# Optimization experiments

Measured on AMD Instinct MI355X. Metric: run time of the kernel, lower is better.

Reference implementation:

```python
import jax, jax.numpy as jnp
import numpy as np

B, H, W, C = 8, 32, 32, 256
HEADS, UNITS = 8, 256
OUT_D = UNITS // HEADS          # 32
HID_D = int(OUT_D * 1.0)        # 32 (hidden_rate=1.0)


def setup_inputs() -> dict:
    key = jax.random.key(0)
    ks = jax.random.split(key, 8)
    glorot_qk = np.sqrt(6.0 / (C + HID_D)).astype(np.float32)
    glorot_v = np.sqrt(6.0 / (C + OUT_D)).astype(np.float32)
    return {
        "seq": jax.random.normal(ks[0], (B, H, W, C), dtype=jnp.float32),
        "ctx": jax.random.normal(ks[1], (B, H, W, C), dtype=jnp.float32),
        "Wq": jax.random.uniform(ks[2], (HEADS, C, HID_D), jnp.float32, -glorot_qk, glorot_qk),
        "Wk": jax.random.uniform(ks[3], (HEADS, C, HID_D), jnp.float32, -glorot_qk, glorot_qk),
        "Wv": jax.random.uniform(ks[4], (HEADS, C, OUT_D), jnp.float32, -glorot_v, glorot_v),
        "bq": jnp.zeros((HEADS, HID_D), jnp.float32),
        "bk": jnp.zeros((HEADS, HID_D), jnp.float32),
        "bv": jnp.zeros((HEADS, OUT_D), jnp.float32),
    }


def reference(seq, ctx, Wq, Wk, Wv, bq, bk, bv):
    # NB: the original layer computes q, k, v all from `seq`; `ctx` only fixes
    # the weight shapes. Dropout omitted (inference / deterministic baseline).
    b, h, w, c = seq.shape
    n = h * w
    s = seq.reshape(b, n, c)
    q = jnp.einsum("bnc,hcd->bhnd", s, Wq) + bq[None, :, None, :]
    k = jnp.einsum("bnc,hcd->bhnd", s, Wk) + bk[None, :, None, :]
    v = jnp.einsum("bnc,hcd->bhnd", s, Wv) + bv[None, :, None, :]
    scale = 1.0 / jnp.sqrt(jnp.asarray(k.shape[-1], k.dtype))
    logits = jnp.einsum("bhnd,bhmd->bhnm", q, k * scale)  # [B,heads,N,N]
    attn = jax.nn.softmax(logits, axis=-1)
    a = jnp.einsum("bhnm,bhmd->bhnd", attn, jnp.tanh(v))  # tanh on V, as in source
    out = a.transpose(0, 2, 1, 3).reshape(b, h, w, -1)     # concat heads on channel
    return out
```

## Files before the change

kernel.cpp:

```cpp
#include <hip/hip_runtime.h>
#include <hip/hip_bf16.h>

typedef __attribute__((ext_vector_type(8))) short bf16x8_t;
typedef __attribute__((ext_vector_type(4))) float f32x4_t;
typedef __attribute__((ext_vector_type(16))) float f32x16_t;
typedef __attribute__((ext_vector_type(4))) unsigned short u16x4_t;
typedef __attribute__((ext_vector_type(2))) unsigned u32x2_t;

#define DEVINL __device__ __forceinline__

static constexpr int CN   = 256;
static constexpr int NSEQ = 1024;
static constexpr int NH   = 8;
static constexpr float QSCALE = 0.17677669529663687f * 1.4426950408889634f;

DEVINL unsigned short f2bf(float f) {
    union { __hip_bfloat16 h; unsigned short u; } cv;
    cv.h = __float2bfloat16(f);
    return cv.u;
}

DEVINL unsigned cvtpk_bf16(float lo, float hi) {
    unsigned r;
    asm("v_cvt_pk_bf16_f32 %0, %1, %2" : "=v"(r) : "v"(lo), "v"(hi));
    return r;
}

DEVINL float partner32_f(float x, int h2) {
    unsigned u = __builtin_bit_cast(unsigned, x);
    u32x2_t r = __builtin_amdgcn_permlane32_swap(u, u, false, false);
    return __builtin_bit_cast(float, h2 ? r.x : r.y);
}

DEVINL float fast_tanh(float x) {
    x = fminf(fmaxf(x, -20.f), 20.f);
    float t = __builtin_amdgcn_exp2f(2.8853900817779268f * x);
    return (t - 1.f) * __builtin_amdgcn_rcpf(t + 1.f);
}

__global__ void prep_kernel(const float* __restrict__ Wq, const float* __restrict__ Wk,
                            const float* __restrict__ Wv, const float* __restrict__ seq,
                            unsigned short* __restrict__ Wbt, unsigned short* __restrict__ Sb) {
    if (blockIdx.x < 768) {
        int idx  = blockIdx.x * 256 + threadIdx.x;
        int c    = idx & 255;
        int ncol = idx >> 8;
        int h = ncol / 96, r = ncol % 96;
        int t = r >> 5, d = r & 31;
        const float* W = (t == 0) ? Wq : (t == 1) ? Wk : Wv;
        Wbt[idx] = f2bf(W[((h << 8) + c) * 32 + d]);
    } else {
        int i = (blockIdx.x - 768) * 256 + threadIdx.x;
        const float4 x = ((const float4*)seq)[2 * i];
        const float4 y = ((const float4*)seq)[2 * i + 1];
        union { unsigned u[4]; bf16x8_t v8; } rv;
        rv.u[0] = cvtpk_bf16(x.x, x.y);
        rv.u[1] = cvtpk_bf16(x.z, x.w);
        rv.u[2] = cvtpk_bf16(y.x, y.y);
        rv.u[3] = cvtpk_bf16(y.z, y.w);
        *(bf16x8_t*)(Sb + (size_t)i * 8) = rv.v8;
    }
}

__global__ __launch_bounds__(256) void proj_kernel(
        const unsigned short* __restrict__ Sb, const unsigned short* __restrict__ Wbt,
        const float* __restrict__ bq, const float* __restrict__ bk, const float* __restrict__ bv,
        unsigned short* __restrict__ Qs, unsigned short* __restrict__ Kf,
        unsigned short* __restrict__ Vf) {
    const int w    = threadIdx.x >> 6;
    const int lane = threadIdx.x & 63;
    const int l15  = lane & 15, l4 = lane >> 4;
    const int mw = blockIdx.y * 64 + (w >> 1) * 32;
    const int nw = blockIdx.x * 128 + (w & 1) * 64;

    f32x4_t acc[2][4];
    for (int mg = 0; mg < 2; ++mg)
        for (int g = 0; g < 4; ++g)
            acc[mg][g] = (f32x4_t){0.f, 0.f, 0.f, 0.f};

#pragma unroll
    for (int k0 = 0; k0 < CN; k0 += 32) {
        const int kk = k0 + l4 * 8;
        bf16x8_t a[2], b[4];
        for (int mg = 0; mg < 2; ++mg)
            a[mg] = *(const bf16x8_t*)(Sb + (size_t)(mw + mg * 16 + l15) * CN + kk);
        for (int g = 0; g < 4; ++g)
            b[g] = *(const bf16x8_t*)(Wbt + (size_t)(nw + g * 16 + l15) * CN + kk);
        for (int mg = 0; mg < 2; ++mg)
            for (int g = 0; g < 4; ++g)
                acc[mg][g] = __builtin_amdgcn_mfma_f32_16x16x32_bf16(a[mg], b[g], acc[mg][g], 0, 0, 0);
    }

    for (int g = 0; g < 4; ++g) {
        const int ncol = nw + g * 16;
        const int h = ncol / 96, r = ncol % 96;
        const int t = r >> 5;
        const int d = (r & 31) + l15;
        for (int mg = 0; mg < 2; ++mg) {
            const int m0 = mw + mg * 16 + l4 * 4;
            const int b_ = m0 >> 10;
            const int n0 = m0 & 1023;
            const int bh = b_ * NH + h;
            const int kt = n0 >> 5;
            if (t == 2) {
                const float bias = bv[h * 32 + d];
                u16x4_t vs;
                for (int i = 0; i < 4; ++i)
                    vs[i] = f2bf(fast_tanh(acc[mg][g][i] + bias));
                const size_t fidx = ((size_t)(bh * 32 + kt) * 2 + ((n0 >> 4) & 1)) * 64
                                    + d + 32 * ((n0 >> 3) & 1);
                *(u16x4_t*)(Vf + fidx * 8 + (n0 & 7)) = vs;
            } else if (t == 0) {
                const float bias = bq[h * 32 + d];
                for (int i = 0; i < 4; ++i)
                    Qs[((size_t)bh * NSEQ + n0 + i) * 32 + d] = f2bf((acc[mg][g][i] + bias) * QSCALE);
            } else {
                const float bias = bk[h * 32 + d];
                const size_t fbase = (((size_t)(bh * 32 + kt) * 2 + (d >> 4)) * 64
                                      + 32 * ((d >> 3) & 1)) * 8 + (d & 7);
                for (int i = 0; i < 4; ++i)
                    Kf[fbase + (size_t)((n0 + i) & 31) * 8] = f2bf(acc[mg][g][i] + bias);
            }
        }
    }
}

__global__ __launch_bounds__(256, 2) void attn_kernel(
        const unsigned short* __restrict__ Qs, const unsigned short* __restrict__ Kf,
        const unsigned short* __restrict__ Vf, float* __restrict__ out) {
    __shared__ float comb[2][2][64][17];
    const int lane = threadIdx.x & 63;
    const int w    = threadIdx.x >> 6;
    const int l31  = lane & 31;
    const int h2   = lane >> 5;
    const int qsel = w >> 1, ksel = w & 1;
    const int id = blockIdx.x;
    const int bh = (id & 7) + 8 * ((id >> 3) & 7);
    const int qt = id >> 6;
    const int b_ = bh >> 3, h = bh & 7;
    const int qbase = qt * 128 + qsel * 64;

    const unsigned short* Qpa = Qs + ((size_t)bh * NSEQ + qbase + l31) * 32 + h2 * 8;
    const unsigned short* Qpb = Qpa + 32 * 32;
    const bf16x8_t qf0a = *(const bf16x8_t*)(Qpa);
    const bf16x8_t qf1a = *(const bf16x8_t*)(Qpa + 16);
    const bf16x8_t qf0b = *(const bf16x8_t*)(Qpb);
    const bf16x8_t qf1b = *(const bf16x8_t*)(Qpb + 16);

    const unsigned short* Kp = Kf + (size_t)bh * 32768 + ksel * 16384 + lane * 8;
    const unsigned short* Vp = Vf + (size_t)bh * 32768 + ksel * 16384 + lane * 8;

    f32x16_t oa = {0.f,0.f,0.f,0.f,0.f,0.f,0.f,0.f,0.f,0.f,0.f,0.f,0.f,0.f,0.f,0.f};
    f32x16_t ob = {0.f,0.f,0.f,0.f,0.f,0.f,0.f,0.f,0.f,0.f,0.f,0.f,0.f,0.f,0.f,0.f};
    float la = 0.f, lb = 0.f;

    bf16x8_t kf0 = *(const bf16x8_t*)(Kp);
    bf16x8_t kf1 = *(const bf16x8_t*)(Kp + 512);
    bf16x8_t va0 = *(const bf16x8_t*)(Vp);
    bf16x8_t va1 = *(const bf16x8_t*)(Vp + 512);

#pragma unroll
    for (int kt = 0; kt < 16; ++kt) {
        const int ktn = (kt + 1) & 15;
        bf16x8_t nk0 = *(const bf16x8_t*)(Kp + ktn * 1024);
        bf16x8_t nk1 = *(const bf16x8_t*)(Kp + ktn * 1024 + 512);
        bf16x8_t nv0 = *(const bf16x8_t*)(Vp + ktn * 1024);
        bf16x8_t nv1 = *(const bf16x8_t*)(Vp + ktn * 1024 + 512);

        {
            f32x16_t st = {0.f,0.f,0.f,0.f,0.f,0.f,0.f,0.f,0.f,0.f,0.f,0.f,0.f,0.f,0.f,0.f};
            __builtin_amdgcn_s_setprio(1);
            st = __builtin_amdgcn_mfma_f32_32x32x16_bf16(kf0, qf0a, st, 0, 0, 0);
            st = __builtin_amdgcn_mfma_f32_32x32x16_bf16(kf1, qf1a, st, 0, 0, 0);
            __builtin_amdgcn_s_setprio(0);
            float p[16];
#pragma unroll
            for (int r = 0; r < 16; ++r) p[r] = __builtin_amdgcn_exp2f(st[r]);
            float s8[8];
#pragma unroll
            for (int g = 0; g < 8; ++g) s8[g] = p[2 * g] + p[2 * g + 1];
            la += ((s8[0] + s8[1]) + (s8[2] + s8[3])) + ((s8[4] + s8[5]) + (s8[6] + s8[7]));
            unsigned pw[8];
#pragma unroll
            for (int g = 0; g < 8; ++g) pw[g] = cvtpk_bf16(p[2 * g], p[2 * g + 1]);
            u32x2_t s02 = __builtin_amdgcn_permlane32_swap(pw[0], pw[2], false, false);
            u32x2_t s13 = __builtin_amdgcn_permlane32_swap(pw[1], pw[3], false, false);
            u32x2_t s46 = __builtin_amdgcn_permlane32_swap(pw[4], pw[6], false, false);
            u32x2_t s57 = __builtin_amdgcn_permlane32_swap(pw[5], pw[7], false, false);
            union { unsigned u[4]; bf16x8_t v; } pb1, pb2;
            pb1.u[0] = s02.x; pb1.u[1] = s13.x; pb1.u[2] = s02.y; pb1.u[3] = s13.y;
            pb2.u[0] = s46.x; pb2.u[1] = s57.x; pb2.u[2] = s46.y; pb2.u[3] = s57.y;
            __builtin_amdgcn_s_setprio(1);
            oa = __builtin_amdgcn_mfma_f32_32x32x16_bf16(va0, pb1.v, oa, 0, 0, 0);
            oa = __builtin_amdgcn_mfma_f32_32x32x16_bf16(va1, pb2.v, oa, 0, 0, 0);
            __builtin_amdgcn_s_setprio(0);
        }
        {
            f32x16_t st = {0.f,0.f,0.f,0.f,0.f,0.f,0.f,0.f,0.f,0.f,0.f,0.f,0.f,0.f,0.f,0.f};
            __builtin_amdgcn_s_setprio(1);
            st = __builtin_amdgcn_mfma_f32_32x32x16_bf16(kf0, qf0b, st, 0, 0, 0);
            st = __builtin_amdgcn_mfma_f32_32x32x16_bf16(kf1, qf1b, st, 0, 0, 0);
            __builtin_amdgcn_s_setprio(0);
            float p[16];
#pragma unroll
            for (int r = 0; r < 16; ++r) p[r] = __builtin_amdgcn_exp2f(st[r]);
            float s8[8];
#pragma unroll
            for (int g = 0; g < 8; ++g) s8[g] = p[2 * g] + p[2 * g + 1];
            lb += ((s8[0] + s8[1]) + (s8[2] + s8[3])) + ((s8[4] + s8[5]) + (s8[6] + s8[7]));
            unsigned pw[8];
#pragma unroll
            for (int g = 0; g < 8; ++g) pw[g] = cvtpk_bf16(p[2 * g], p[2 * g + 1]);
            u32x2_t s02 = __builtin_amdgcn_permlane32_swap(pw[0], pw[2], false, false);
            u32x2_t s13 = __builtin_amdgcn_permlane32_swap(pw[1], pw[3], false, false);
            u32x2_t s46 = __builtin_amdgcn_permlane32_swap(pw[4], pw[6], false, false);
            u32x2_t s57 = __builtin_amdgcn_permlane32_swap(pw[5], pw[7], false, false);
            union { unsigned u[4]; bf16x8_t v; } pb1, pb2;
            pb1.u[0] = s02.x; pb1.u[1] = s13.x; pb1.u[2] = s02.y; pb1.u[3] = s13.y;
            pb2.u[0] = s46.x; pb2.u[1] = s57.x; pb2.u[2] = s46.y; pb2.u[3] = s57.y;
            __builtin_amdgcn_s_setprio(1);
            ob = __builtin_amdgcn_mfma_f32_32x32x16_bf16(va0, pb1.v, ob, 0, 0, 0);
            ob = __builtin_amdgcn_mfma_f32_32x32x16_bf16(va1, pb2.v, ob, 0, 0, 0);
            __builtin_amdgcn_s_setprio(0);
        }

        kf0 = nk0; kf1 = nk1; va0 = nv0; va1 = nv1;
    }

    const float lha = la + partner32_f(la, h2);
    const float lhb = lb + partner32_f(lb, h2);

    if (ksel) {
#pragma unroll
        for (int r = 0; r < 16; ++r) {
            comb[qsel][0][lane][r] = oa[r];
            comb[qsel][1][lane][r] = ob[r];
        }
        comb[qsel][0][lane][16] = lha;
        comb[qsel][1][lane][16] = lhb;
    }
    __syncthreads();
    if (!ksel) {
        {
            const float* c = comb[qsel][0][lane];
            const float inv = 1.0f / (lha + c[16]);
            float* op = out + ((size_t)(b_ * NSEQ + qbase + l31)) * 256 + h * 32 + h2 * 4;
#pragma unroll
            for (int g = 0; g < 4; ++g) {
                float4 q4;
                q4.x = (oa[4 * g + 0] + c[4 * g + 0]) * inv;
                q4.y = (oa[4 * g + 1] + c[4 * g + 1]) * inv;
                q4.z = (oa[4 * g + 2] + c[4 * g + 2]) * inv;
                q4.w = (oa[4 * g + 3] + c[4 * g + 3]) * inv;
                *(float4*)(op + 8 * g) = q4;
            }
        }
        {
            const float* c = comb[qsel][1][lane];
            const float inv = 1.0f / (lhb + c[16]);
            float* op = out + ((size_t)(b_ * NSEQ + qbase + 32 + l31)) * 256 + h * 32 + h2 * 4;
#pragma unroll
            for (int g = 0; g < 4; ++g) {
                float4 q4;
                q4.x = (ob[4 * g + 0] + c[4 * g + 0]) * inv;
                q4.y = (ob[4 * g + 1] + c[4 * g + 1]) * inv;
                q4.z = (ob[4 * g + 2] + c[4 * g + 2]) * inv;
                q4.w = (ob[4 * g + 3] + c[4 * g + 3]) * inv;
                *(float4*)(op + 8 * g) = q4;
            }
        }
    }
}

extern "C" void kernel_launch(void* const* d_in, const int* in_sizes, int n_in,
                              void* d_out, int out_size, void* d_ws, size_t ws_size,
                              hipStream_t stream) {
    const float* seq = (const float*)d_in[0];
    const float* Wq = (const float*)d_in[2];
    const float* Wk = (const float*)d_in[3];
    const float* Wv = (const float*)d_in[4];
    const float* bq = (const float*)d_in[5];
    const float* bk = (const float*)d_in[6];
    const float* bv = (const float*)d_in[7];
    float* out = (float*)d_out;

    char* ws = (char*)d_ws;
    unsigned short* Wbt = (unsigned short*)ws;
    unsigned short* Qs  = (unsigned short*)(ws + 393216);
    unsigned short* Kf  = (unsigned short*)(ws + 393216 + 4194304);
    unsigned short* Vf  = (unsigned short*)(ws + 393216 + 2 * 4194304);
    unsigned short* Sb  = (unsigned short*)(ws + 393216 + 3 * 4194304);

    hipLaunchKernelGGL(prep_kernel, dim3(1792), dim3(256), 0, stream, Wq, Wk, Wv, seq, Wbt, Sb);
    hipLaunchKernelGGL(proj_kernel, dim3(6, 128), dim3(256), 0, stream,
                       Sb, Wbt, bq, bk, bv, Qs, Kf, Vf);
    hipLaunchKernelGGL(attn_kernel, dim3(512), dim3(256), 0, stream, Qs, Kf, Vf, out);
}
```

Before: 45.83 us.

## Fuse bf16 conversion of weights and inputs into the projection kernel

Removes the separate prep kernel. Each projection block now converts its 128-column weight slice to bf16 and stages it in LDS, and converts the fp32 sequence tile to bf16 in registers right before the MFMA. This drops one kernel launch and the write and re-read of the bf16 workspace copies. In exchange, every block redoes the weight conversion with strided global reads, the fp32 input is read once per column block, and the larger LDS footprint may lower occupancy.

```diff
diff --git a/kernel.cpp b/kernel.cpp
--- a/kernel.cpp
+++ b/kernel.cpp
@@ -38,40 +38,33 @@
     return (t - 1.f) * __builtin_amdgcn_rcpf(t + 1.f);
 }
 
-__global__ void prep_kernel(const float* __restrict__ Wq, const float* __restrict__ Wk,
-                            const float* __restrict__ Wv, const float* __restrict__ seq,
-                            unsigned short* __restrict__ Wbt, unsigned short* __restrict__ Sb) {
-    if (blockIdx.x < 768) {
-        int idx  = blockIdx.x * 256 + threadIdx.x;
-        int c    = idx & 255;
-        int ncol = idx >> 8;
-        int h = ncol / 96, r = ncol % 96;
-        int t = r >> 5, d = r & 31;
-        const float* W = (t == 0) ? Wq : (t == 1) ? Wk : Wv;
-        Wbt[idx] = f2bf(W[((h << 8) + c) * 32 + d]);
-    } else {
-        int i = (blockIdx.x - 768) * 256 + threadIdx.x;
-        const float4 x = ((const float4*)seq)[2 * i];
-        const float4 y = ((const float4*)seq)[2 * i + 1];
-        union { unsigned u[4]; bf16x8_t v8; } rv;
-        rv.u[0] = cvtpk_bf16(x.x, x.y);
-        rv.u[1] = cvtpk_bf16(x.z, x.w);
-        rv.u[2] = cvtpk_bf16(y.x, y.y);
-        rv.u[3] = cvtpk_bf16(y.z, y.w);
-        *(bf16x8_t*)(Sb + (size_t)i * 8) = rv.v8;
-    }
-}
-
 __global__ __launch_bounds__(256) void proj_kernel(
-        const unsigned short* __restrict__ Sb, const unsigned short* __restrict__ Wbt,
+        const float* __restrict__ seq,
+        const float* __restrict__ Wq, const float* __restrict__ Wk, const float* __restrict__ Wv,
         const float* __restrict__ bq, const float* __restrict__ bk, const float* __restrict__ bv,
         unsigned short* __restrict__ Qs, unsigned short* __restrict__ Kf,
         unsigned short* __restrict__ Vf) {
-    const int w    = threadIdx.x >> 6;
-    const int lane = threadIdx.x & 63;
+    __shared__ __attribute__((aligned(16))) unsigned short Wl[128][264];
+    const int id   = blockIdx.x;
+    const int by   = id & 127, bx = id >> 7;
+    const int tid  = threadIdx.x;
+    const int w    = tid >> 6;
+    const int lane = tid & 63;
     const int l15  = lane & 15, l4 = lane >> 4;
-    const int mw = blockIdx.y * 64 + (w >> 1) * 32;
-    const int nw = blockIdx.x * 128 + (w & 1) * 64;
+    const int mw = by * 64 + (w >> 1) * 32;
+    const int nw = bx * 128 + (w & 1) * 64;
+
+    {
+        const int ncol0 = bx * 128;
+        int h = ncol0 / 96, r = ncol0 % 96;
+        for (int c = 0; c < 128; ++c) {
+            const int t = r >> 5, d = r & 31;
+            const float* Wsrc = (t == 0) ? Wq : (t == 1) ? Wk : Wv;
+            Wl[c][tid] = f2bf(Wsrc[(size_t)h * 8192 + tid * 32 + d]);
+            if (++r == 96) { r = 0; ++h; }
+        }
+    }
+    __syncthreads();
 
     f32x4_t acc[2][4];
     for (int mg = 0; mg < 2; ++mg)
@@ -82,10 +75,19 @@
     for (int k0 = 0; k0 < CN; k0 += 32) {
         const int kk = k0 + l4 * 8;
         bf16x8_t a[2], b[4];
-        for (int mg = 0; mg < 2; ++mg)
-            a[mg] = *(const bf16x8_t*)(Sb + (size_t)(mw + mg * 16 + l15) * CN + kk);
+        for (int mg = 0; mg < 2; ++mg) {
+            const float* p = seq + (size_t)(mw + mg * 16 + l15) * CN + kk;
+            const float4 x = *(const float4*)p;
+            const float4 y = *(const float4*)(p + 4);
+            union { unsigned u[4]; bf16x8_t v; } av;
+            av.u[0] = cvtpk_bf16(x.x, x.y);
+            av.u[1] = cvtpk_bf16(x.z, x.w);
+            av.u[2] = cvtpk_bf16(y.x, y.y);
+            av.u[3] = cvtpk_bf16(y.z, y.w);
+            a[mg] = av.v;
+        }
         for (int g = 0; g < 4; ++g)
-            b[g] = *(const bf16x8_t*)(Wbt + (size_t)(nw + g * 16 + l15) * CN + kk);
+            b[g] = *(const bf16x8_t*)(&Wl[(w & 1) * 64 + g * 16 + l15][kk]);
         for (int mg = 0; mg < 2; ++mg)
             for (int g = 0; g < 4; ++g)
                 acc[mg][g] = __builtin_amdgcn_mfma_f32_16x16x32_bf16(a[mg], b[g], acc[mg][g], 0, 0, 0);
@@ -285,14 +287,11 @@
     float* out = (float*)d_out;
 
     char* ws = (char*)d_ws;
-    unsigned short* Wbt = (unsigned short*)ws;
-    unsigned short* Qs  = (unsigned short*)(ws + 393216);
-    unsigned short* Kf  = (unsigned short*)(ws + 393216 + 4194304);
-    unsigned short* Vf  = (unsigned short*)(ws + 393216 + 2 * 4194304);
-    unsigned short* Sb  = (unsigned short*)(ws + 393216 + 3 * 4194304);
-
-    hipLaunchKernelGGL(prep_kernel, dim3(1792), dim3(256), 0, stream, Wq, Wk, Wv, seq, Wbt, Sb);
-    hipLaunchKernelGGL(proj_kernel, dim3(6, 128), dim3(256), 0, stream,
-                       Sb, Wbt, bq, bk, bv, Qs, Kf, Vf);
+    unsigned short* Qs = (unsigned short*)ws;
+    unsigned short* Kf = (unsigned short*)(ws + 4194304);
+    unsigned short* Vf = (unsigned short*)(ws + 2 * 4194304);
+
+    hipLaunchKernelGGL(proj_kernel, dim3(768), dim3(256), 0, stream,
+                       seq, Wq, Wk, Wv, bq, bk, bv, Qs, Kf, Vf);
     hipLaunchKernelGGL(attn_kernel, dim3(512), dim3(256), 0, stream, Qs, Kf, Vf, out);
 }
```

After: 95.47 us. +108.3%, slower.
